# Optimization experiments

Hardware: AMD Instinct MI355X
Metric: run time of the kernel (lower is better)

Reference implementation:

```python
import jax, jax.numpy as jnp
import numpy as np

B, S, D, H, DFF = 2, 2048, 1024, 16, 4096
DK = D // H
EPS = 1e-6


def layer_norm(x, alpha, bias):
    # torch: alpha * (x - mean) / (std_unbiased + eps) + bias
    mean = jnp.mean(x, axis=-1, keepdims=True)
    std = jnp.sqrt(jnp.var(x, axis=-1, keepdims=True, ddof=1))
    return alpha * (x - mean) / (std + EPS) + bias


def setup_inputs() -> dict:
    key = jax.random.key(0)
    ks = jax.random.split(key, 10)
    w = lambda k, shape: (jax.random.normal(k, shape, jnp.float32) * 0.02)
    return {
        "x": jax.random.normal(ks[0], (B, S, D), jnp.float32),
        "mask": jnp.ones((B, 1, 1, S), jnp.int32),
        "wq": w(ks[1], (D, D)),
        "wk": w(ks[2], (D, D)),
        "wv": w(ks[3], (D, D)),
        "wo": w(ks[4], (D, D)),
        "w1": w(ks[5], (DFF, D)),
        "b1": jnp.zeros((DFF,), jnp.float32),
        "w2": w(ks[6], (D, DFF)),
        "b2": jnp.zeros((D,), jnp.float32),
        "alpha1": jnp.ones((D,), jnp.float32),
        "bias1": jnp.zeros((D,), jnp.float32),
        "alpha2": jnp.ones((D,), jnp.float32),
        "bias2": jnp.zeros((D,), jnp.float32),
    }


def reference(x, mask, wq, wk, wv, wo, w1, b1, w2, b2, alpha1, bias1, alpha2, bias2):
    # --- residual 1: pre-norm + self-attention ---
    xn = layer_norm(x, alpha1, bias1)                      # [B,S,D]
    q = (xn @ wq.T).reshape(B, S, H, DK).transpose(0, 2, 1, 3)  # [B,H,S,DK]
    k = (xn @ wk.T).reshape(B, S, H, DK).transpose(0, 2, 1, 3)
    v = (xn @ wv.T).reshape(B, S, H, DK).transpose(0, 2, 1, 3)
    scores = jnp.einsum("bhqd,bhkd->bhqk", q, k) / jnp.sqrt(jnp.float32(DK))
    scores = jnp.where(mask == 0, jnp.float32(-1e9), scores)
    attn = jax.nn.softmax(scores, axis=-1)                 # [B,H,S,S]
    av = jnp.einsum("bhqk,bhkd->bhqd", attn, v)            # [B,H,S,DK]
    av = av.transpose(0, 2, 1, 3).reshape(B, S, D)
    x = x + av @ wo.T                                      # dropout p=0
    # --- residual 2: pre-norm + FFN ---
    xn2 = layer_norm(x, alpha2, bias2)
    h = jax.nn.relu(xn2 @ w1.T + b1)                       # [B,S,DFF]
    x = x + h @ w2.T + b2
    return x
```

## Files before the change

kernel.cpp:

```cpp
#include <hip/hip_runtime.h>

#define B_   2
#define S_   2048
#define D_   1024
#define H_   16
#define DK_  64
#define DFF_ 4096
#define NTOK (B_ * S_)

#define QSCALE 0.18033688011112042f

typedef __bf16 bf16x8 __attribute__((ext_vector_type(8)));
typedef __bf16 bf16x4 __attribute__((ext_vector_type(4)));
typedef float  f32x4  __attribute__((ext_vector_type(4)));

#if __has_builtin(__builtin_amdgcn_exp2f)
#define EXP2(x) __builtin_amdgcn_exp2f(x)
#else
#define EXP2(x) exp2f(x)
#endif

__device__ __forceinline__ void ld16(const __bf16* g, __bf16* l) {
  __builtin_amdgcn_global_load_lds(
      (const __attribute__((address_space(1))) void*)g,
      (__attribute__((address_space(3))) void*)l, 16, 0, 0);
}

#define RAW_BAR()     __asm__ __volatile__("s_barrier" ::: "memory")
#define SCHED_FENCE() __builtin_amdgcn_sched_barrier(0)

__device__ __forceinline__ void xcd_swizzle(int& bx, int& by) {
  const int gx = gridDim.x;
  const int flat = blockIdx.y * gx + blockIdx.x;
  const int x = flat & 7;
  const int n = flat >> 3;
  if (gx == 32) {
    const int px = (x & 1) << 4, py = (x >> 1) << 3;
    const int g = n >> 5, rem = n & 31;
    bx = px + (g << 2) + (rem & 3);
    by = py + (rem >> 2);
  } else {
    const int g = n >> 4, rem = n & 15;
    bx = (g << 2) + (rem & 3);
    by = (x << 2) + (rem >> 2);
  }
}

__device__ __forceinline__ void xcd_swz256(int& bx, int& by) {
  const int gx = gridDim.x;
  const int flat = blockIdx.y * gx + blockIdx.x;
  const int x = flat & 7, n = flat >> 3;
  if (gx == 16) { by = ((x >> 1) << 2) + (n >> 3); bx = ((x & 1) << 3) + (n & 7); }
  else          { by = (x << 1) + (n >> 2);        bx = n & 3; }
}

__device__ __forceinline__ void lda4(bf16x8 (&afr)[4], const __bf16* hb,
                                     int abase, int f0) {
#pragma unroll
  for (int i = 0; i < 4; ++i)
    afr[i] = *(const bf16x8*)(hb + abase + (f0 + i) * 512);
}

__device__ __forceinline__ void ldb4(bf16x8 (&bfr)[4], const __bf16* hb,
                                     int bbase) {
#pragma unroll
  for (int j = 0; j < 4; ++j)
    bfr[j] = *(const bf16x8*)(hb + bbase + j * 512);
}

__device__ __forceinline__ void mm16(f32x4 (&acc)[8][4], const bf16x8 (&afr)[4],
                                     const bf16x8 (&bfr)[4], int r0) {
#pragma unroll
  for (int i = 0; i < 4; ++i)
#pragma unroll
    for (int j = 0; j < 4; ++j)
      acc[r0 + i][j] =
          __builtin_amdgcn_mfma_f32_16x16x32_bf16(afr[i], bfr[j], acc[r0 + i][j], 0, 0, 0);
}

__device__ __forceinline__ void gemm_core_256(
    const __bf16* __restrict__ A, const __bf16* __restrict__ W,
    int ld, int kLen, int rowA0, int rowW0,
    f32x4 (&acc)[8][4], __bf16* Ls)
{
  const int t = threadIdx.x;
  const int lane = t & 63, wv = t >> 6;
  const int wm = wv >> 2, wn = wv & 3;
  const int l15 = lane & 15, q4 = lane >> 4;

  const int lane_rd = l15 * 32 + ((q4 * 8) ^ (((l15 >> 1) & 3) << 3));
  const int abase = wm * 4096 + lane_rd;
  const int bbase = wn * 2048 + lane_rd;

  const int sc0 = t ^ ((t >> 3) & 3);
  const __bf16* gA0 = A + (size_t)(rowA0 + (sc0 >> 2)) * ld + (sc0 & 3) * 8;
  const __bf16* gA1 = gA0 + (size_t)128 * ld;
  const __bf16* gW0 = W + (size_t)(rowW0 + (sc0 >> 2)) * ld + (sc0 & 3) * 8;
  const __bf16* gW1 = gW0 + (size_t)128 * ld;
  const int d0 = wv * 512, d1 = 4096 + wv * 512;

#pragma unroll
  for (int i = 0; i < 8; ++i)
#pragma unroll
    for (int j = 0; j < 4; ++j) acc[i][j] = (f32x4){0.f, 0.f, 0.f, 0.f};

#define HBASE(slot, mat, h) (Ls + ((((slot)*2) + (mat)) * 2 + (h)) * 8192)
#define STG_A(tt, h, slot) do { __bf16* _d = HBASE(slot, 0, h);              \
    const int _ko = (tt) * 64 + (h) * 32;                                    \
    ld16(gA0 + _ko, _d + d0); ld16(gA1 + _ko, _d + d1); } while (0)
#define STG_B(tt, h, slot) do { __bf16* _d = HBASE(slot, 1, h);              \
    const int _ko = (tt) * 64 + (h) * 32;                                    \
    ld16(gW0 + _ko, _d + d0); ld16(gW1 + _ko, _d + d1); } while (0)
#define MFMA_PH(r0) do { RAW_BAR(); SCHED_FENCE();                           \
    __builtin_amdgcn_s_setprio(1); mm16(acc, afr, bfr, r0);                  \
    __builtin_amdgcn_s_setprio(0); SCHED_FENCE(); RAW_BAR(); } while (0)

  const int NT = kLen >> 6;
  bf16x8 afr[4], bfr[4];

  STG_A(0, 0, 0); STG_A(0, 1, 0); STG_B(0, 0, 0); STG_B(0, 1, 0);
  STG_B(1, 0, 1); STG_A(1, 0, 1); STG_B(1, 1, 1);
  __asm__ __volatile__("s_waitcnt vmcnt(6)" ::: "memory");
  RAW_BAR(); SCHED_FENCE();

  for (int u = 0; u < NT; u += 2) {
    const bool g2 = (u + 2) < NT, g3 = (u + 3) < NT;
    lda4(afr, HBASE(0, 0, 0), abase, 0); ldb4(bfr, HBASE(0, 1, 0), bbase);
    STG_A(u + 1, 1, 1);
    MFMA_PH(0);
    lda4(afr, HBASE(0, 0, 0), abase, 4);
    if (g2) STG_B(u + 2, 0, 0);
    MFMA_PH(4);
    lda4(afr, HBASE(0, 0, 1), abase, 0); ldb4(bfr, HBASE(0, 1, 1), bbase);
    if (g2) STG_A(u + 2, 0, 0);
    MFMA_PH(0);
    lda4(afr, HBASE(0, 0, 1), abase, 4);
    if (g2) {
      STG_B(u + 2, 1, 0);
      __asm__ __volatile__("s_waitcnt vmcnt(6)" ::: "memory");
    } else {
      __asm__ __volatile__("s_waitcnt vmcnt(0)" ::: "memory");
    }
    MFMA_PH(4);
    lda4(afr, HBASE(1, 0, 0), abase, 0); ldb4(bfr, HBASE(1, 1, 0), bbase);
    if (g2) STG_A(u + 2, 1, 0);
    MFMA_PH(0);
    lda4(afr, HBASE(1, 0, 0), abase, 4);
    if (g3) STG_B(u + 3, 0, 1);
    MFMA_PH(4);
    lda4(afr, HBASE(1, 0, 1), abase, 0); ldb4(bfr, HBASE(1, 1, 1), bbase);
    if (g3) STG_A(u + 3, 0, 1);
    MFMA_PH(0);
    lda4(afr, HBASE(1, 0, 1), abase, 4);
    if (g3) STG_B(u + 3, 1, 1);
    __asm__ __volatile__("s_waitcnt vmcnt(6)" ::: "memory");
    MFMA_PH(4);
  }
#undef HBASE
#undef STG_A
#undef STG_B
#undef MFMA_PH
}

__device__ __forceinline__ void gemm_core_128(
    const __bf16* __restrict__ A, const __bf16* __restrict__ W,
    int ld, int kLen, int rowA0, int rowW0,
    f32x4 (&acc)[4][4], __bf16* As, __bf16* Bs)
{
  const int t    = threadIdx.x;
  const int lane = t & 63;
  const int wv   = t >> 6;
  const int wm   = (wv >> 1) << 6;
  const int wn   = (wv & 1) << 6;
  const int l15  = lane & 15;
  const int q4   = lane >> 4;

#pragma unroll
  for (int i = 0; i < 4; ++i)
#pragma unroll
    for (int j = 0; j < 4; ++j)
      acc[i][j] = (f32x4){0.f, 0.f, 0.f, 0.f};

  const __bf16* gA = A + (size_t)(rowA0 + 32 * wv + l15) * ld + q4 * 8;
  const __bf16* gW = W + (size_t)(rowW0 + 32 * wv + l15) * ld + q4 * 8;
  __bf16* lA = As + wv * 2048;
  __bf16* lB = Bs + wv * 2048;
  const size_t r16 = (size_t)16 * ld;

  const int fbg = (q4 << 7) + (l15 << 3);
  const int ia = (wm >> 4);
  const int ib = (wn >> 4);

  for (int k0 = 0; k0 < kLen; k0 += 64) {
    ld16(gA + k0,            lA);
    ld16(gA + k0 + 32,       lA + 512);
    ld16(gA + k0 + r16,      lA + 1024);
    ld16(gA + k0 + r16 + 32, lA + 1536);
    ld16(gW + k0,            lB);
    ld16(gW + k0 + 32,       lB + 512);
    ld16(gW + k0 + r16,      lB + 1024);
    ld16(gW + k0 + r16 + 32, lB + 1536);
    __syncthreads();
#pragma unroll
    for (int s = 0; s < 2; ++s) {
      bf16x8 af[4], bw[4];
#pragma unroll
      for (int i = 0; i < 4; ++i)
        af[i] = *(const bf16x8*)(As + (ia + i) * 1024 + s * 512 + fbg);
#pragma unroll
      for (int j = 0; j < 4; ++j)
        bw[j] = *(const bf16x8*)(Bs + (ib + j) * 1024 + s * 512 + fbg);
#pragma unroll
      for (int i = 0; i < 4; ++i)
#pragma unroll
        for (int j = 0; j < 4; ++j)
          acc[i][j] = __builtin_amdgcn_mfma_f32_16x16x32_bf16(af[i], bw[j], acc[i][j], 0, 0, 0);
    }
    __syncthreads();
  }
}

__global__ __launch_bounds__(512, 2) void gemm_qkv_256(
    const __bf16* __restrict__ xn,
    const __bf16* __restrict__ wqb, const __bf16* __restrict__ wkb,
    const __bf16* __restrict__ wvb,
    __bf16* __restrict__ qo, __bf16* __restrict__ ko, __bf16* __restrict__ vto)
{
  __shared__ __align__(16) __bf16 Ls[65536];
  int bx, by; xcd_swz256(bx, by);
  const __bf16* W = blockIdx.z == 0 ? wqb : (blockIdx.z == 1 ? wkb : wvb);
  f32x4 acc[8][4];
  gemm_core_256(xn, W, D_, D_, by * 256, bx * 256, acc, Ls);

  const int t = threadIdx.x, lane = t & 63, wv = t >> 6;
  const int wm = wv >> 2, wn = wv & 3;
  const int l15 = lane & 15, q4 = lane >> 4;
  const int row0 = by * 256 + wm * 128;
  const int col0 = bx * 256 + wn * 64;

  if (blockIdx.z < 2) {
    __bf16* o = blockIdx.z == 0 ? qo : ko;
    const float sc = blockIdx.z == 0 ? QSCALE : 1.0f;
#pragma unroll
    for (int fr = 0; fr < 8; ++fr)
#pragma unroll
      for (int fc = 0; fc < 4; ++fc) {
        const int col = col0 + fc * 16 + l15;
#pragma unroll
        for (int r = 0; r < 4; ++r) {
          const int row = row0 + fr * 16 + q4 * 4 + r;
          o[(size_t)row * D_ + col] = (__bf16)(acc[fr][fc][r] * sc);
        }
      }
  } else {
#pragma unroll
    for (int fr = 0; fr < 8; ++fr)
#pragma unroll
      for (int fc = 0; fc < 4; ++fc) {
        const int tok0 = row0 + fr * 16 + q4 * 4;
        const int c    = col0 + fc * 16 + l15;
        const int b0 = tok0 >> 11, s0 = tok0 & (S_ - 1);
        const int hh = c >> 6, dd = c & (DK_ - 1);
        bf16x4 pk;
#pragma unroll
        for (int r = 0; r < 4; ++r) pk[r] = (__bf16)acc[fr][fc][r];
        *(bf16x4*)&vto[(size_t)((b0 * H_ + hh) * DK_ + dd) * S_ + s0] = pk;
      }
  }
}

__global__ __launch_bounds__(512, 2) void gemm_ffn1_256(
    const __bf16* __restrict__ A, const __bf16* __restrict__ W,
    __bf16* __restrict__ outb, const float* __restrict__ bias)
{
  __shared__ __align__(16) __bf16 Ls[65536];
  int bx, by; xcd_swz256(bx, by);
  f32x4 acc[8][4];
  gemm_core_256(A, W, D_, D_, by * 256, bx * 256, acc, Ls);

  const int t = threadIdx.x, lane = t & 63, wv = t >> 6;
  const int wm = wv >> 2, wn = wv & 3;
  const int l15 = lane & 15, q4 = lane >> 4;
  const int row0 = by * 256 + wm * 128;
  const int col0 = bx * 256 + wn * 64;

#pragma unroll
  for (int fr = 0; fr < 8; ++fr)
#pragma unroll
    for (int fc = 0; fc < 4; ++fc) {
      const int col = col0 + fc * 16 + l15;
      const float bs = bias[col];
#pragma unroll
      for (int r = 0; r < 4; ++r) {
        const int row = row0 + fr * 16 + q4 * 4 + r;
        outb[(size_t)row * DFF_ + col] = (__bf16)fmaxf(acc[fr][fc][r] + bs, 0.0f);
      }
    }
}

__global__ __launch_bounds__(512, 2) void gemm_ffn2_sk4(
    const __bf16* __restrict__ A, const __bf16* __restrict__ W,
    __bf16* __restrict__ pp)
{
  __shared__ __align__(16) __bf16 Ls[65536];
  int bx, by; xcd_swz256(bx, by);
  const int z = blockIdx.z;
  f32x4 acc[8][4];
  gemm_core_256(A + (size_t)z * 1024, W + (size_t)z * 1024, DFF_, 1024,
                by * 256, bx * 256, acc, Ls);

  const int t = threadIdx.x, lane = t & 63, wv = t >> 6;
  const int wm = wv >> 2, wn = wv & 3;
  const int l15 = lane & 15, q4 = lane >> 4;
  const int row0 = by * 256 + wm * 128;
  const int col0 = bx * 256 + wn * 64;
  __bf16* out = pp + (size_t)z * NTOK * D_;

#pragma unroll
  for (int fr = 0; fr < 8; ++fr)
#pragma unroll
    for (int fc = 0; fc < 4; ++fc) {
      const int col = col0 + fc * 16 + l15;
#pragma unroll
      for (int r = 0; r < 4; ++r) {
        const int row = row0 + fr * 16 + q4 * 4 + r;
        out[(size_t)row * D_ + col] = (__bf16)acc[fr][fc][r];
      }
    }
}

__global__ __launch_bounds__(256) void gemm_splitk_f32(
    const __bf16* __restrict__ A, const __bf16* __restrict__ W,
    int K, int kPart, float* __restrict__ pp)
{
  __shared__ __align__(16) __bf16 As[128 * 64];
  __shared__ __align__(16) __bf16 Bs[128 * 64];
  int bx, by; xcd_swizzle(bx, by);
  f32x4 acc[4][4];
  const int z = blockIdx.z;
  gemm_core_128(A + (size_t)z * kPart, W + (size_t)z * kPart, K, kPart,
                by * 128, bx * 128, acc, As, Bs);

  const int t = threadIdx.x, lane = t & 63, wv = t >> 6;
  const int wm = (wv >> 1) << 6, wn = (wv & 1) << 6;
  const int l15 = lane & 15, q4 = lane >> 4;
  const int row0 = by * 128 + wm;
  const int col0 = bx * 128 + wn;
  float* out = pp + (size_t)z * NTOK * D_;

#pragma unroll
  for (int i = 0; i < 4; ++i)
#pragma unroll
    for (int j = 0; j < 4; ++j)
#pragma unroll
      for (int r = 0; r < 4; ++r) {
        int row = row0 + 16 * i + q4 * 4 + r;
        int col = col0 + 16 * j + l15;
        out[(size_t)row * D_ + col] = acc[i][j][r];
      }
}

__global__ __launch_bounds__(256) void oproj_ln_reduce(
    const float* __restrict__ x, const float* __restrict__ p0,
    const float* __restrict__ p1, const float* __restrict__ alpha,
    const float* __restrict__ bias, float* __restrict__ x1,
    __bf16* __restrict__ xn2)
{
  const int row = blockIdx.x;
  const int t = threadIdx.x;
  const size_t base = (size_t)row * D_;
  float4 v  = ((const float4*)(x  + base))[t];
  const float4 a0 = ((const float4*)(p0 + base))[t];
  const float4 a1 = ((const float4*)(p1 + base))[t];
  v.x += a0.x + a1.x; v.y += a0.y + a1.y;
  v.z += a0.z + a1.z; v.w += a0.w + a1.w;
  ((float4*)(x1 + base))[t] = v;

  float s  = v.x + v.y + v.z + v.w;
  float ss = v.x * v.x + v.y * v.y + v.z * v.z + v.w * v.w;
#pragma unroll
  for (int m = 1; m < 64; m <<= 1) {
    s  += __shfl_xor(s, m);
    ss += __shfl_xor(ss, m);
  }
  __shared__ float red[8];
  if ((t & 63) == 0) { red[t >> 6] = s; red[4 + (t >> 6)] = ss; }
  __syncthreads();
  s  = red[0] + red[1] + red[2] + red[3];
  ss = red[4] + red[5] + red[6] + red[7];
  const float mean = s * (1.0f / D_);
  float var = (ss - (float)D_ * mean * mean) * (1.0f / (D_ - 1));
  var = fmaxf(var, 0.0f);
  const float inv = 1.0f / (sqrtf(var) + 1e-6f);
  const float4 al = ((const float4*)alpha)[t];
  const float4 bi = ((const float4*)bias)[t];
  bf16x4 o;
  o.x = (__bf16)(al.x * (v.x - mean) * inv + bi.x);
  o.y = (__bf16)(al.y * (v.y - mean) * inv + bi.y);
  o.z = (__bf16)(al.z * (v.z - mean) * inv + bi.z);
  o.w = (__bf16)(al.w * (v.w - mean) * inv + bi.w);
  ((bf16x4*)(xn2 + base))[t] = o;
}

__global__ __launch_bounds__(256) void ffn2_reduce(
    const float* __restrict__ x1, const __bf16* __restrict__ pp,
    const float* __restrict__ b2, float* __restrict__ out)
{
  const int idx4 = blockIdx.x * 256 + threadIdx.x;
  float4 v = ((const float4*)x1)[idx4];
  const float4 bs = ((const float4*)b2)[idx4 & 255];
  const size_t st = (size_t)NTOK * D_ / 4;
  const bf16x4 q0 = ((const bf16x4*)pp)[idx4];
  const bf16x4 q1 = ((const bf16x4*)pp)[idx4 + st];
  const bf16x4 q2 = ((const bf16x4*)pp)[idx4 + 2 * st];
  const bf16x4 q3 = ((const bf16x4*)pp)[idx4 + 3 * st];
  v.x += bs.x + (float)q0[0] + (float)q1[0] + (float)q2[0] + (float)q3[0];
  v.y += bs.y + (float)q0[1] + (float)q1[1] + (float)q2[1] + (float)q3[1];
  v.z += bs.z + (float)q0[2] + (float)q1[2] + (float)q2[2] + (float)q3[2];
  v.w += bs.w + (float)q0[3] + (float)q1[3] + (float)q2[3] + (float)q3[3];
  ((float4*)out)[idx4] = v;
}

struct CastJobs {
  const float* src[6];
  __bf16* dst[6];
  int n4[6];
};

__global__ __launch_bounds__(256) void cast_ln_kernel(
    CastJobs cj, const float* __restrict__ x, const float* __restrict__ alpha,
    const float* __restrict__ bias, __bf16* __restrict__ xn1)
{
  const int j = blockIdx.y;
  if (j < 6) {
    const int i = blockIdx.x * 256 + threadIdx.x;
    if (i < cj.n4[j]) {
      float4 v = ((const float4*)cj.src[j])[i];
      bf16x4 o;
      o.x = (__bf16)v.x; o.y = (__bf16)v.y; o.z = (__bf16)v.z; o.w = (__bf16)v.w;
      ((bf16x4*)cj.dst[j])[i] = o;
    }
    return;
  }
  const int row = blockIdx.x;
  const int t = threadIdx.x;
  const float4 v = ((const float4*)(x + (size_t)row * D_))[t];
  float s  = v.x + v.y + v.z + v.w;
  float ss = v.x * v.x + v.y * v.y + v.z * v.z + v.w * v.w;
#pragma unroll
  for (int m = 1; m < 64; m <<= 1) {
    s  += __shfl_xor(s, m);
    ss += __shfl_xor(ss, m);
  }
  __shared__ float red[8];
  if ((t & 63) == 0) { red[t >> 6] = s; red[4 + (t >> 6)] = ss; }
  __syncthreads();
  s  = red[0] + red[1] + red[2] + red[3];
  ss = red[4] + red[5] + red[6] + red[7];
  const float mean = s * (1.0f / D_);
  float var = (ss - (float)D_ * mean * mean) * (1.0f / (D_ - 1));
  var = fmaxf(var, 0.0f);
  const float inv = 1.0f / (sqrtf(var) + 1e-6f);
  const float4 al = ((const float4*)alpha)[t];
  const float4 bi = ((const float4*)bias)[t];
  bf16x4 o;
  o.x = (__bf16)(al.x * (v.x - mean) * inv + bi.x);
  o.y = (__bf16)(al.y * (v.y - mean) * inv + bi.y);
  o.z = (__bf16)(al.z * (v.z - mean) * inv + bi.z);
  o.w = (__bf16)(al.w * (v.w - mean) * inv + bi.w);
  ((bf16x4*)(xn1 + (size_t)row * D_))[t] = o;
}

__global__ __launch_bounds__(256) void attn_kernel(
    const __bf16* __restrict__ qg, const __bf16* __restrict__ kg,
    const __bf16* __restrict__ vtg, const int* __restrict__ mask,
    __bf16* __restrict__ av)
{
  __shared__ __align__(16) __bf16 Ks[2][64 * 64];
  __shared__ __align__(16) __bf16 Vt[2][64 * 64];
  __shared__ __align__(16) __bf16 Ps[128 * 72];
  __shared__ int Dd[32];

  const int t = threadIdx.x, lane = t & 63, wv = t >> 6;
  const int l15 = lane & 15, q4 = lane >> 4;
  const int bh = blockIdx.x;
  const int b = bh >> 4, h = bh & (H_ - 1);
  const int q0 = blockIdx.y * 128;

  const int srow = lane & 7, sc8 = lane >> 3;
  const __bf16* qg0 = qg + (size_t)(b * S_ + q0 + 32 * wv + srow) * D_ + h * DK_ + sc8 * 8;
  __bf16* lQ = Ps + wv * 2304;
#pragma unroll
  for (int p = 0; p < 4; ++p)
    ld16(qg0 + (size_t)(8 * p) * D_, lQ + 512 * p);

  const __bf16* kg0 = kg + (size_t)(b * S_ + 16 * wv + srow) * D_ + h * DK_ + sc8 * 8;
  const __bf16* vt0 = vtg + (size_t)(bh * DK_ + 16 * wv + srow) * S_ + sc8 * 8;

  if (t < 32) Dd[t] = 0;

  ld16(kg0,                  Ks[0] + wv * 1024);
  ld16(kg0 + (size_t)8 * D_, Ks[0] + wv * 1024 + 512);
  ld16(vt0,                  Vt[0] + wv * 1024);
  ld16(vt0 + (size_t)8 * S_, Vt[0] + wv * 1024 + 512);

  __syncthreads();

  {
    const int4* m4 = (const int4*)(mask + (size_t)b * S_) + t * 2;
    const int4 a = m4[0], c = m4[1];
    const bool anyz = (a.x == 0) | (a.y == 0) | (a.z == 0) | (a.w == 0) |
                      (c.x == 0) | (c.y == 0) | (c.z == 0) | (c.w == 0);
    if (anyz) Dd[t >> 3] = 1;
  }
  __syncthreads();

  const int fb = ((l15 >> 3) << 9) + (q4 << 6) + ((l15 & 7) << 3);
  const int mrow = b * S_;

  bf16x8 bq[2][2];
#pragma unroll
  for (int j = 0; j < 2; ++j)
#pragma unroll
    for (int s = 0; s < 2; ++s)
      bq[j][s] = *(const bf16x8*)(lQ + j * 1024 + s * 256 + fb);

  float lsum[2] = {0.0f, 0.0f};
  f32x4 oacc[2][4];
#pragma unroll
  for (int m = 0; m < 2; ++m)
#pragma unroll
    for (int jd = 0; jd < 4; ++jd) oacc[m][jd] = (f32x4){0.f, 0.f, 0.f, 0.f};

  for (int kv0 = 0; kv0 < S_; kv0 += 64) {
    const int buf = (kv0 >> 6) & 1;
    if (kv0 + 64 < S_) {
      const size_t nk = (size_t)(kv0 + 64);
      ld16(kg0 + nk * D_,              Ks[buf ^ 1] + wv * 1024);
      ld16(kg0 + (nk + 8) * D_,        Ks[buf ^ 1] + wv * 1024 + 512);
      ld16(vt0 + nk,                   Vt[buf ^ 1] + wv * 1024);
      ld16(vt0 + (size_t)8 * S_ + nk,  Vt[buf ^ 1] + wv * 1024 + 512);
    }

    f32x4 sacc[4][2];
#pragma unroll
    for (int i = 0; i < 4; ++i)
#pragma unroll
      for (int j = 0; j < 2; ++j) sacc[i][j] = (f32x4){0.f, 0.f, 0.f, 0.f};
    __builtin_amdgcn_s_setprio(1);
#pragma unroll
    for (int i = 0; i < 4; ++i)
#pragma unroll
      for (int s = 0; s < 2; ++s) {
        bf16x8 ak = *(const bf16x8*)(Ks[buf] + i * 1024 + fb + s * 256);
#pragma unroll
        for (int j = 0; j < 2; ++j)
          sacc[i][j] = __builtin_amdgcn_mfma_f32_16x16x32_bf16(ak, bq[j][s], sacc[i][j], 0, 0, 0);
      }
    __builtin_amdgcn_s_setprio(0);

    if (Dd[kv0 >> 6]) {
#pragma unroll
      for (int i = 0; i < 4; ++i)
#pragma unroll
        for (int r = 0; r < 4; ++r)
          if (mask[mrow + kv0 + 16 * i + 4 * q4 + r] == 0) {
            sacc[i][0][r] = -1e30f;
            sacc[i][1][r] = -1e30f;
          }
    }

#pragma unroll
    for (int j = 0; j < 2; ++j) {
      float rs = 0.0f;
#pragma unroll
      for (int i = 0; i < 4; ++i) {
        bf16x4 pb;
#pragma unroll
        for (int r = 0; r < 4; ++r) {
          float pp = EXP2(sacc[i][j][r]);
          rs += pp;
          pb[r] = (__bf16)pp;
        }
        *(bf16x4*)(Ps + (wv * 32 + j * 16 + l15) * 72 + 16 * i + q4 * 4) = pb;
      }
      lsum[j] += rs;
    }

    bf16x8 ap[2][2];
#pragma unroll
    for (int m = 0; m < 2; ++m)
#pragma unroll
      for (int s = 0; s < 2; ++s)
        ap[m][s] = *(const bf16x8*)(Ps + (wv * 32 + 16 * m + l15) * 72 + s * 32 + q4 * 8);
    __builtin_amdgcn_s_setprio(1);
#pragma unroll
    for (int jd = 0; jd < 4; ++jd)
#pragma unroll
      for (int s = 0; s < 2; ++s) {
        bf16x8 bv = *(const bf16x8*)(Vt[buf] + jd * 1024 + fb + s * 256);
#pragma unroll
        for (int m = 0; m < 2; ++m)
          oacc[m][jd] = __builtin_amdgcn_mfma_f32_16x16x32_bf16(ap[m][s], bv, oacc[m][jd], 0, 0, 0);
      }
    __builtin_amdgcn_s_setprio(0);

    __syncthreads();
  }

#pragma unroll
  for (int j = 0; j < 2; ++j) {
    lsum[j] += __shfl_xor(lsum[j], 16);
    lsum[j] += __shfl_xor(lsum[j], 32);
  }
  float lt[2][4];
#pragma unroll
  for (int m = 0; m < 2; ++m)
#pragma unroll
    for (int r = 0; r < 4; ++r) lt[m][r] = 1.0f / __shfl(lsum[m], q4 * 4 + r);
#pragma unroll
  for (int m = 0; m < 2; ++m)
#pragma unroll
    for (int jd = 0; jd < 4; ++jd)
#pragma unroll
      for (int r = 0; r < 4; ++r) {
        int tok = b * S_ + q0 + wv * 32 + 16 * m + q4 * 4 + r;
        int c   = h * DK_ + jd * 16 + l15;
        av[(size_t)tok * D_ + c] = (__bf16)(oacc[m][jd][r] * lt[m][r]);
      }
}

extern "C" void kernel_launch(void* const* d_in, const int* in_sizes, int n_in,
                              void* d_out, int out_size, void* d_ws, size_t ws_size,
                              hipStream_t stream) {
  const float* x      = (const float*)d_in[0];
  const int*   mask   = (const int*)d_in[1];
  const float* wq     = (const float*)d_in[2];
  const float* wk     = (const float*)d_in[3];
  const float* wv     = (const float*)d_in[4];
  const float* wo     = (const float*)d_in[5];
  const float* w1     = (const float*)d_in[6];
  const float* b1     = (const float*)d_in[7];
  const float* w2     = (const float*)d_in[8];
  const float* b2     = (const float*)d_in[9];
  const float* alpha1 = (const float*)d_in[10];
  const float* bias1  = (const float*)d_in[11];
  const float* alpha2 = (const float*)d_in[12];
  const float* bias2  = (const float*)d_in[13];

  char* ws = (char*)d_ws;
  __bf16* wqb = (__bf16*)(ws + ((size_t)0 << 20));
  __bf16* wkb = (__bf16*)(ws + ((size_t)2 << 20));
  __bf16* wvb = (__bf16*)(ws + ((size_t)4 << 20));
  __bf16* wob = (__bf16*)(ws + ((size_t)6 << 20));
  __bf16* w1b = (__bf16*)(ws + ((size_t)8 << 20));
  __bf16* w2b = (__bf16*)(ws + ((size_t)16 << 20));
  __bf16* xn1 = (__bf16*)(ws + ((size_t)24 << 20));
  __bf16* qb  = (__bf16*)(ws + ((size_t)32 << 20));
  __bf16* kb  = (__bf16*)(ws + ((size_t)40 << 20));
  __bf16* vtb = (__bf16*)(ws + ((size_t)48 << 20));
  __bf16* avb = (__bf16*)(ws + ((size_t)56 << 20));
  float*  x1  = (float*) (ws + ((size_t)64 << 20));
  __bf16* xn2 = (__bf16*)(ws + ((size_t)56 << 20));
  __bf16* hb  = (__bf16*)(ws + ((size_t)24 << 20));
  float*  op0 = (float*) (ws + ((size_t)24 << 20));
  float*  op1 = (float*) (ws + ((size_t)40 << 20));
  __bf16* fpp = (__bf16*)(ws + ((size_t)32 << 20));

  CastJobs cj;
  cj.src[0] = wq; cj.dst[0] = wqb; cj.n4[0] = D_ * D_ / 4;
  cj.src[1] = wk; cj.dst[1] = wkb; cj.n4[1] = D_ * D_ / 4;
  cj.src[2] = wv; cj.dst[2] = wvb; cj.n4[2] = D_ * D_ / 4;
  cj.src[3] = wo; cj.dst[3] = wob; cj.n4[3] = D_ * D_ / 4;
  cj.src[4] = w1; cj.dst[4] = w1b; cj.n4[4] = DFF_ * D_ / 4;
  cj.src[5] = w2; cj.dst[5] = w2b; cj.n4[5] = DFF_ * D_ / 4;

  cast_ln_kernel<<<dim3(DFF_ * D_ / 4 / 256, 7), 256, 0, stream>>>(
      cj, x, alpha1, bias1, xn1);

  gemm_qkv_256<<<dim3(D_ / 256, NTOK / 256, 3), 512, 0, stream>>>(
      xn1, wqb, wkb, wvb, qb, kb, vtb);

  attn_kernel<<<dim3(B_ * H_, S_ / 128), 256, 0, stream>>>(qb, kb, vtb, mask, avb);

  gemm_splitk_f32<<<dim3(D_ / 128, NTOK / 128, 2), 256, 0, stream>>>(
      avb, wob, D_, D_ / 2, op0);

  oproj_ln_reduce<<<dim3(NTOK), 256, 0, stream>>>(
      x, op0, op1, alpha2, bias2, x1, xn2);

  gemm_ffn1_256<<<dim3(DFF_ / 256, NTOK / 256), 512, 0, stream>>>(
      xn2, w1b, hb, b1);

  gemm_ffn2_sk4<<<dim3(D_ / 256, NTOK / 256, 4), 512, 0, stream>>>(
      hb, w2b, fpp);

  ffn2_reduce<<<dim3(NTOK * D_ / 4 / 256), 256, 0, stream>>>(
      x1, fpp, b2, (float*)d_out);
}
```

Measured before the change: 326.1 us.

## Use 256-tile GEMM for output projection; compute softmax row sums via MFMA

Result: slower. 332.6 us (+2.0%).

```diff
diff --git a/kernel.cpp b/kernel.cpp
--- a/kernel.cpp
+++ b/kernel.cpp
@@ -28,23 +28,6 @@
 
 #define RAW_BAR()     __asm__ __volatile__("s_barrier" ::: "memory")
 #define SCHED_FENCE() __builtin_amdgcn_sched_barrier(0)
-
-__device__ __forceinline__ void xcd_swizzle(int& bx, int& by) {
-  const int gx = gridDim.x;
-  const int flat = blockIdx.y * gx + blockIdx.x;
-  const int x = flat & 7;
-  const int n = flat >> 3;
-  if (gx == 32) {
-    const int px = (x & 1) << 4, py = (x >> 1) << 3;
-    const int g = n >> 5, rem = n & 31;
-    bx = px + (g << 2) + (rem & 3);
-    by = py + (rem >> 2);
-  } else {
-    const int g = n >> 4, rem = n & 15;
-    bx = (g << 2) + (rem & 3);
-    by = (x << 2) + (rem >> 2);
-  }
-}
 
 __device__ __forceinline__ void xcd_swz256(int& bx, int& by) {
   const int gx = gridDim.x;
@@ -162,64 +145,6 @@
 #undef MFMA_PH
 }
 
-__device__ __forceinline__ void gemm_core_128(
-    const __bf16* __restrict__ A, const __bf16* __restrict__ W,
-    int ld, int kLen, int rowA0, int rowW0,
-    f32x4 (&acc)[4][4], __bf16* As, __bf16* Bs)
-{
-  const int t    = threadIdx.x;
-  const int lane = t & 63;
-  const int wv   = t >> 6;
-  const int wm   = (wv >> 1) << 6;
-  const int wn   = (wv & 1) << 6;
-  const int l15  = lane & 15;
-  const int q4   = lane >> 4;
-
-#pragma unroll
-  for (int i = 0; i < 4; ++i)
-#pragma unroll
-    for (int j = 0; j < 4; ++j)
-      acc[i][j] = (f32x4){0.f, 0.f, 0.f, 0.f};
-
-  const __bf16* gA = A + (size_t)(rowA0 + 32 * wv + l15) * ld + q4 * 8;
-  const __bf16* gW = W + (size_t)(rowW0 + 32 * wv + l15) * ld + q4 * 8;
-  __bf16* lA = As + wv * 2048;
-  __bf16* lB = Bs + wv * 2048;
-  const size_t r16 = (size_t)16 * ld;
-
-  const int fbg = (q4 << 7) + (l15 << 3);
-  const int ia = (wm >> 4);
-  const int ib = (wn >> 4);
-
-  for (int k0 = 0; k0 < kLen; k0 += 64) {
-    ld16(gA + k0,            lA);
-    ld16(gA + k0 + 32,       lA + 512);
-    ld16(gA + k0 + r16,      lA + 1024);
-    ld16(gA + k0 + r16 + 32, lA + 1536);
-    ld16(gW + k0,            lB);
-    ld16(gW + k0 + 32,       lB + 512);
-    ld16(gW + k0 + r16,      lB + 1024);
-    ld16(gW + k0 + r16 + 32, lB + 1536);
-    __syncthreads();
-#pragma unroll
-    for (int s = 0; s < 2; ++s) {
-      bf16x8 af[4], bw[4];
-#pragma unroll
-      for (int i = 0; i < 4; ++i)
-        af[i] = *(const bf16x8*)(As + (ia + i) * 1024 + s * 512 + fbg);
-#pragma unroll
-      for (int j = 0; j < 4; ++j)
-        bw[j] = *(const bf16x8*)(Bs + (ib + j) * 1024 + s * 512 + fbg);
-#pragma unroll
-      for (int i = 0; i < 4; ++i)
-#pragma unroll
-        for (int j = 0; j < 4; ++j)
-          acc[i][j] = __builtin_amdgcn_mfma_f32_16x16x32_bf16(af[i], bw[j], acc[i][j], 0, 0, 0);
-    }
-    __syncthreads();
-  }
-}
-
 __global__ __launch_bounds__(512, 2) void gemm_qkv_256(
     const __bf16* __restrict__ xn,
     const __bf16* __restrict__ wqb, const __bf16* __restrict__ wkb,
@@ -329,35 +254,35 @@
     }
 }
 
-__global__ __launch_bounds__(256) void gemm_splitk_f32(
+__global__ __launch_bounds__(512, 2) void gemm_oproj_256(
     const __bf16* __restrict__ A, const __bf16* __restrict__ W,
-    int K, int kPart, float* __restrict__ pp)
-{
-  __shared__ __align__(16) __bf16 As[128 * 64];
-  __shared__ __align__(16) __bf16 Bs[128 * 64];
-  int bx, by; xcd_swizzle(bx, by);
-  f32x4 acc[4][4];
+    float* __restrict__ p0, float* __restrict__ p1)
+{
+  __shared__ __align__(16) __bf16 Ls[65536];
+  int bx, by; xcd_swz256(bx, by);
   const int z = blockIdx.z;
-  gemm_core_128(A + (size_t)z * kPart, W + (size_t)z * kPart, K, kPart,
-                by * 128, bx * 128, acc, As, Bs);
+  f32x4 acc[8][4];
+  gemm_core_256(A + (size_t)z * 512, W + (size_t)z * 512, D_, 512,
+                by * 256, bx * 256, acc, Ls);
 
   const int t = threadIdx.x, lane = t & 63, wv = t >> 6;
-  const int wm = (wv >> 1) << 6, wn = (wv & 1) << 6;
+  const int wm = wv >> 2, wn = wv & 3;
   const int l15 = lane & 15, q4 = lane >> 4;
-  const int row0 = by * 128 + wm;
-  const int col0 = bx * 128 + wn;
-  float* out = pp + (size_t)z * NTOK * D_;
-
-#pragma unroll
-  for (int i = 0; i < 4; ++i)
-#pragma unroll
-    for (int j = 0; j < 4; ++j)
+  const int row0 = by * 256 + wm * 128;
+  const int col0 = bx * 256 + wn * 64;
+  float* out = z == 0 ? p0 : p1;
+
+#pragma unroll
+  for (int fr = 0; fr < 8; ++fr)
+#pragma unroll
+    for (int fc = 0; fc < 4; ++fc) {
+      const int col = col0 + fc * 16 + l15;
 #pragma unroll
       for (int r = 0; r < 4; ++r) {
-        int row = row0 + 16 * i + q4 * 4 + r;
-        int col = col0 + 16 * j + l15;
-        out[(size_t)row * D_ + col] = acc[i][j][r];
-      }
+        const int row = row0 + fr * 16 + q4 * 4 + r;
+        out[(size_t)row * D_ + col] = acc[fr][fc][r];
+      }
+    }
 }
 
 __global__ __launch_bounds__(256) void oproj_ln_reduce(
@@ -514,6 +439,7 @@
     if (anyz) Dd[t >> 3] = 1;
   }
   __syncthreads();
+  const bool blockDirty = (__ballot(Dd[lane & 31] != 0) != 0ull);
 
   const int fb = ((l15 >> 3) << 9) + (q4 << 6) + ((l15 & 7) << 3);
   const int mrow = b * S_;
@@ -525,12 +451,18 @@
     for (int s = 0; s < 2; ++s)
       bq[j][s] = *(const bf16x8*)(lQ + j * 1024 + s * 256 + fb);
 
-  float lsum[2] = {0.0f, 0.0f};
+  bf16x8 bones;
+#pragma unroll
+  for (int e = 0; e < 8; ++e) bones[e] = (__bf16)1.0f;
+
+  f32x4 lacc[2];
   f32x4 oacc[2][4];
 #pragma unroll
-  for (int m = 0; m < 2; ++m)
+  for (int m = 0; m < 2; ++m) {
+    lacc[m] = (f32x4){0.f, 0.f, 0.f, 0.f};
 #pragma unroll
     for (int jd = 0; jd < 4; ++jd) oacc[m][jd] = (f32x4){0.f, 0.f, 0.f, 0.f};
+  }
 
   for (int kv0 = 0; kv0 < S_; kv0 += 64) {
     const int buf = (kv0 >> 6) & 1;
@@ -559,7 +491,7 @@
       }
     __builtin_amdgcn_s_setprio(0);
 
-    if (Dd[kv0 >> 6]) {
+    if (blockDirty && Dd[kv0 >> 6]) {
 #pragma unroll
       for (int i = 0; i < 4; ++i)
 #pragma unroll
@@ -571,21 +503,14 @@
     }
 
 #pragma unroll
-    for (int j = 0; j < 2; ++j) {
-      float rs = 0.0f;
+    for (int j = 0; j < 2; ++j)
 #pragma unroll
       for (int i = 0; i < 4; ++i) {
         bf16x4 pb;
 #pragma unroll
-        for (int r = 0; r < 4; ++r) {
-          float pp = EXP2(sacc[i][j][r]);
-          rs += pp;
-          pb[r] = (__bf16)pp;
-        }
+        for (int r = 0; r < 4; ++r) pb[r] = (__bf16)EXP2(sacc[i][j][r]);
         *(bf16x4*)(Ps + (wv * 32 + j * 16 + l15) * 72 + 16 * i + q4 * 4) = pb;
       }
-      lsum[j] += rs;
-    }
 
     bf16x8 ap[2][2];
 #pragma unroll
@@ -603,31 +528,30 @@
         for (int m = 0; m < 2; ++m)
           oacc[m][jd] = __builtin_amdgcn_mfma_f32_16x16x32_bf16(ap[m][s], bv, oacc[m][jd], 0, 0, 0);
       }
+#pragma unroll
+    for (int m = 0; m < 2; ++m)
+#pragma unroll
+      for (int s = 0; s < 2; ++s)
+        lacc[m] = __builtin_amdgcn_mfma_f32_16x16x32_bf16(ap[m][s], bones, lacc[m], 0, 0, 0);
     __builtin_amdgcn_s_setprio(0);
 
     __syncthreads();
   }
 
 #pragma unroll
-  for (int j = 0; j < 2; ++j) {
-    lsum[j] += __shfl_xor(lsum[j], 16);
-    lsum[j] += __shfl_xor(lsum[j], 32);
-  }
-  float lt[2][4];
-#pragma unroll
-  for (int m = 0; m < 2; ++m)
-#pragma unroll
-    for (int r = 0; r < 4; ++r) lt[m][r] = 1.0f / __shfl(lsum[m], q4 * 4 + r);
-#pragma unroll
-  for (int m = 0; m < 2; ++m)
+  for (int m = 0; m < 2; ++m) {
+    f32x4 lt;
+#pragma unroll
+    for (int r = 0; r < 4; ++r) lt[r] = 1.0f / lacc[m][r];
 #pragma unroll
     for (int jd = 0; jd < 4; ++jd)
 #pragma unroll
       for (int r = 0; r < 4; ++r) {
         int tok = b * S_ + q0 + wv * 32 + 16 * m + q4 * 4 + r;
         int c   = h * DK_ + jd * 16 + l15;
-        av[(size_t)tok * D_ + c] = (__bf16)(oacc[m][jd][r] * lt[m][r]);
-      }
+        av[(size_t)tok * D_ + c] = (__bf16)(oacc[m][jd][r] * lt[r]);
+      }
+  }
 }
 
 extern "C" void kernel_launch(void* const* d_in, const int* in_sizes, int n_in,
@@ -683,8 +607,8 @@
 
   attn_kernel<<<dim3(B_ * H_, S_ / 128), 256, 0, stream>>>(qb, kb, vtb, mask, avb);
 
-  gemm_splitk_f32<<<dim3(D_ / 128, NTOK / 128, 2), 256, 0, stream>>>(
-      avb, wob, D_, D_ / 2, op0);
+  gemm_oproj_256<<<dim3(D_ / 256, NTOK / 256, 2), 512, 0, stream>>>(
+      avb, wob, op0, op1);
 
   oproj_ln_reduce<<<dim3(NTOK), 256, 0, stream>>>(
       x, op0, op1, alpha2, bias2, x1, xn2);
```
